# Optimization experiments

Measured on AMD Instinct MI355X. Metric: run time of the kernel, lower is better.

The kernel has to match this reference:

```python
import jax, jax.numpy as jnp
from jax import lax
import numpy as np

L, G, C = 4, 2, 4  # num_blocks, num_sparsity_groups, num_sparsity_cardinals
IMAGE_MEAN = 0.5
SCALE = 2


def _wn(v, g):
    # weight_norm over dims (1,2,3), g per output channel
    n = jnp.sqrt(jnp.sum(v * v, axis=(1, 2, 3), keepdims=True))
    return (g.reshape(-1, 1, 1, 1) / n) * v


def _conv(x, w, b, pad):
    y = lax.conv_general_dilated(x, w, (1, 1), [(pad, pad), (pad, pad)],
                                 dimension_numbers=('NCHW', 'OIHW', 'NCHW'))
    return y + b[None, :, None, None]


def _dyn_conv(x, v, g, b, mw, mb):
    # sparsity-routed conv: per-sample expert mixture of kernels
    w = _wn(v, g)                                   # [G*out, in, k, k]
    B = x.shape[0]
    logits = x.mean((-1, -2)) @ mw.T + mb           # [B, G*C]
    s = jax.nn.softmax(logits.reshape(B, G, C), axis=1)
    wv = w.reshape(G, C, -1, *w.shape[1:])          # [G, C, D, in, k, k]
    wper = jnp.einsum('bgc,gcdikl->bcdikl', s, wv)
    wper = wper.reshape(B, -1, *w.shape[1:])        # [B, out, in, k, k]
    bper = jnp.einsum('bgc,gcd->bcd', s, b.reshape(G, C, -1)).reshape(B, -1)

    def per_sample(xi, wi, bi):
        yi = lax.conv_general_dilated(xi[None], wi, (1, 1), [(1, 1), (1, 1)],
                                      dimension_numbers=('NCHW', 'OIHW', 'NCHW'))[0]
        return yi + bi[:, None, None]

    return jax.vmap(per_sample)(x, wper, bper)


def _pixel_shuffle(x, r):
    B, Cc, H, W = x.shape
    x = x.reshape(B, Cc // (r * r), r, r, H, W)
    x = x.transpose(0, 1, 4, 2, 5, 3)
    return x.reshape(B, Cc // (r * r), H * r, W * r)


def setup_inputs() -> dict:
    key = jax.random.key(0)
    ks = jax.random.split(key, 16)
    f32 = jnp.float32
    inp = {
        'x': jax.random.uniform(ks[0], (8, 3, 64, 64), dtype=f32),
        'head_v': jax.random.normal(ks[1], (64, 3, 3, 3), dtype=f32) * 0.05,
        'head_g': jnp.ones((64,), f32),
        'head_b': jnp.zeros((64,), f32),
        'b1_v': jax.random.normal(ks[2], (L, 512, 64, 3, 3), dtype=f32) * 0.05,
        'b1_g': jnp.full((L, 512), 2.0, f32),
        'b1_b': jnp.zeros((L, 512), f32),
        'b1_mw': jax.random.normal(ks[3], (L, 8, 64), dtype=f32) * 0.05,
        'b1_mb': jax.random.normal(ks[4], (L, 8), dtype=f32) * 0.05,
        'b2_v': jax.random.normal(ks[5], (L, 128, 256, 3, 3), dtype=f32) * 0.05,
        'b2_g': jnp.full((L, 128), 1.0 / np.sqrt(L), f32),
        'b2_b': jnp.zeros((L, 128), f32),
        'b2_mw': jax.random.normal(ks[6], (L, 8, 256), dtype=f32) * 0.05,
        'b2_mb': jax.random.normal(ks[7], (L, 8), dtype=f32) * 0.05,
        'tail_v': jax.random.normal(ks[8], (12, 64, 3, 3), dtype=f32) * 0.05,
        'tail_g': jnp.ones((12,), f32),
        'tail_b': jnp.zeros((12,), f32),
        'skip_v': jax.random.normal(ks[9], (12, 3, 5, 5), dtype=f32) * 0.05,
        'skip_g': jnp.ones((12,), f32),
        'skip_b': jnp.zeros((12,), f32),
    }
    return inp


def reference(x, head_v, head_g, head_b,
              b1_v, b1_g, b1_b, b1_mw, b1_mb,
              b2_v, b2_g, b2_b, b2_mw, b2_mb,
              tail_v, tail_g, tail_b,
              skip_v, skip_g, skip_b):
    x = x - IMAGE_MEAN
    h = _conv(x, _wn(head_v, head_g), head_b, pad=1)
    for l in range(L):
        r0 = h
        t = _dyn_conv(h, b1_v[l], b1_g[l], b1_b[l], b1_mw[l], b1_mb[l])
        t = jax.nn.relu(t)
        t = _dyn_conv(t, b2_v[l], b2_g[l], b2_b[l], b2_mw[l], b2_mb[l])
        h = t + r0
    body = _conv(h, _wn(tail_v, tail_g), tail_b, pad=1)
    s = _conv(x, _wn(skip_v, skip_g), skip_b, pad=2)
    y = _pixel_shuffle(body + s, SCALE) + IMAGE_MEAN
    return y
```

## Files before the change

### kernel.cpp

```cpp
#include <hip/hip_runtime.h>

typedef __attribute__((ext_vector_type(8))) short bf16x8;
typedef __attribute__((ext_vector_type(4))) float f32x4;
typedef __attribute__((ext_vector_type(8))) unsigned short u16x8;

__device__ __forceinline__ unsigned short bf16u(float x) {
    unsigned int u = __builtin_bit_cast(unsigned int, x);
    unsigned int r = (u + 0x7fffu + ((u >> 16) & 1u)) >> 16;
    return (unsigned short)r;
}
__device__ __forceinline__ float bf2f(unsigned short u) {
    return __builtin_bit_cast(float, (unsigned int)u << 16);
}
__device__ __forceinline__ void gll16(const void* g, void* l) {
    __builtin_amdgcn_global_load_lds((const __attribute__((address_space(1))) void*)g,
                                     (__attribute__((address_space(3))) void*)l, 16, 0, 0);
}

__global__ __launch_bounds__(256) void setup_kernel(
    unsigned short* __restrict__ hbf, unsigned short* __restrict__ tbf,
    float* __restrict__ sums,
    const float* __restrict__ hv, const float* __restrict__ hg, float* __restrict__ hw,
    const float* __restrict__ kv, const float* __restrict__ kg, float* __restrict__ kw) {
    int blk = blockIdx.x;
    if (blk < 335) {
        int i = blk * 256 + threadIdx.x;
        u16x8 z8 = {0, 0, 0, 0, 0, 0, 0, 0};
        if (i < 16640) {
            int chv = i & 3, pb = i >> 2, pos = pb % 260, bc = pb / 260;
            int y, x;
            if (pos < 66) { y = 0; x = pos; }
            else if (pos < 132) { y = 65; x = pos - 66; }
            else if (pos < 196) { y = pos - 131; x = 0; }
            else { y = pos - 195; x = 65; }
            *(u16x8*)&hbf[((size_t)bc * 4356 + y * 66 + x) * 32 + chv * 8] = z8;
        } else if (i < 83200) {
            int j = i - 16640;
            int chv = j & 3, pb = j >> 2, pos = pb % 260, bc = pb / 260;
            int y, x;
            if (pos < 66) { y = 0; x = pos; }
            else if (pos < 132) { y = 65; x = pos - 66; }
            else if (pos < 196) { y = pos - 131; x = 0; }
            else { y = pos - 195; x = 65; }
            *(u16x8*)&tbf[((size_t)bc * 4356 + y * 66 + x) * 32 + chv * 8] = z8;
        } else {
            int k = i - 83200;
            f32x4 z4 = {0.f, 0.f, 0.f, 0.f};
            ((f32x4*)sums)[k] = z4;
        }
        return;
    }
    int b2 = blk - 335;
    const float *v, *g;
    float* outw;
    int len, row;
    if (b2 < 64) { v = hv; g = hg; outw = hw; len = 27; row = b2; }
    else         { v = kv; g = kg; outw = kw; len = 75; row = b2 - 64; }
    __shared__ float red[4];
    __shared__ float s_sc;
    const float* vr = v + (size_t)row * len;
    float ss = 0.f;
    for (int i = threadIdx.x; i < len; i += 256) { float a = vr[i]; ss += a * a; }
    for (int o = 32; o > 0; o >>= 1) ss += __shfl_down(ss, o);
    if ((threadIdx.x & 63) == 0) red[threadIdx.x >> 6] = ss;
    __syncthreads();
    if (threadIdx.x == 0) s_sc = g[row] / sqrtf(red[0] + red[1] + red[2] + red[3]);
    __syncthreads();
    float sc = s_sc;
    float* orow = outw + (size_t)row * len;
    for (int i = threadIdx.x; i < len; i += 256) orow[i] = vr[i] * sc;
}

__global__ __launch_bounds__(256) void tail_repack2(const float* __restrict__ tv,
                                                    const float* __restrict__ tg,
                                                    unsigned short* __restrict__ wq) {
    __shared__ float row[576];
    __shared__ float red[4];
    __shared__ float s_sc;
    int mo = blockIdx.x;
    int tid = threadIdx.x;
    if (mo < 12) {
        for (int i = tid; i < 576; i += 256) row[i] = tv[mo * 576 + i];
        __syncthreads();
        float ss = 0.f;
        for (int i = tid; i < 576; i += 256) { float a = row[i]; ss += a * a; }
        for (int o = 32; o > 0; o >>= 1) ss += __shfl_down(ss, o);
        if ((tid & 63) == 0) red[tid >> 6] = ss;
        __syncthreads();
        if (tid == 0) s_sc = tg[mo] / sqrtf(red[0] + red[1] + red[2] + red[3]);
        __syncthreads();
        float sc = s_sc;
        for (int ch = tid; ch < 72; ch += 256) {
            int kg = ch & 3, c2 = ch >> 2;
            int t = c2 % 9, kc = c2 / 9;
            u16x8 pk;
#pragma unroll
            for (int kj = 0; kj < 8; ++kj) {
                int ic = kc * 32 + kg * 8 + kj;
                pk[kj] = bf16u(row[ic * 9 + t] * sc);
            }
            *(u16x8*)&wq[(size_t)((kc * 9 + t) * 4 + kg) * 128 + mo * 8] = pk;
        }
    } else {
        u16x8 z = {0, 0, 0, 0, 0, 0, 0, 0};
        for (int ch = tid; ch < 72; ch += 256) {
            int kg = ch & 3, c2 = ch >> 2;
            int t = c2 % 9, kc = c2 / 9;
            *(u16x8*)&wq[(size_t)((kc * 9 + t) * 4 + kg) * 128 + mo * 8] = z;
        }
    }
}

template <int IC, int GOC, int LGMO>
__global__ __launch_bounds__(256) void combine_v4(
    const float* __restrict__ v, const float* __restrict__ g,
    const float* __restrict__ msum, const float* __restrict__ mw,
    const float* __restrict__ mb, float* __restrict__ s_out,
    unsigned short* __restrict__ wq, int D, int OC) {
    constexpr int ROWF = IC * 9;
    constexpr int KCh = IC / 32;
    constexpr int ROWS2 = 2 * GOC;
    constexpr int TOTC = GOC * KCh * 9 * 4;
    constexpr int TPR = 256 / ROWS2;
    __shared__ float lv[ROWS2 * ROWF];
    __shared__ float lg[8], sv8[8], scr[ROWS2], sw[ROWS2];
    int tid = threadIdx.x;
    int ocg = blockIdx.x * GOC;
    int b = blockIdx.y;
    for (int i = tid; i < ROWS2 * ROWF; i += 256) {
        int r = i / ROWF, jj = i - r * ROWF;
        int oc_r = (r / GOC) * OC + ocg + (r % GOC);
        lv[i] = v[(size_t)oc_r * ROWF + jj];
    }
    {
        int j = tid >> 5, l32 = tid & 31;
        float part = 0.f;
        for (int i = l32; i < IC; i += 32) part += msum[b * IC + i] * mw[j * IC + i];
        for (int m = 16; m > 0; m >>= 1) part += __shfl_xor(part, m);
        if (l32 == 0) lg[j] = part * (1.f / 4096.f) + mb[j];
    }
    __syncthreads();
    {
        int r = tid / TPR, lr = tid % TPR;
        float ss = 0.f;
        for (int i = lr; i < ROWF; i += TPR) { float a = lv[r * ROWF + i]; ss += a * a; }
#pragma unroll
        for (int m = TPR >> 1; m > 0; m >>= 1) ss += __shfl_xor(ss, m);
        if (lr == 0) {
            int oc_r = (r / GOC) * OC + ocg + (r % GOC);
            scr[r] = g[oc_r] / sqrtf(ss);
        }
    }
    if (tid < 8) {
        int gg = tid >> 2, c = tid & 3;
        float l0 = lg[c], l1 = lg[4 + c];
        float m = fmaxf(l0, l1);
        float e0 = __expf(l0 - m), e1 = __expf(l1 - m);
        float val = ((gg == 0) ? e0 : e1) / (e0 + e1);
        sv8[tid] = val;
        if (blockIdx.x == 0) s_out[b * 8 + tid] = val;
    }
    __syncthreads();
    if (tid < ROWS2) {
        int r = tid;
        int oc = ocg + (r % GOC);
        int cd = oc / D;
        float s = (r < GOC) ? sv8[cd] : sv8[4 + cd];
        sw[r] = s * scr[r];
    }
    __syncthreads();
    for (int ci = tid; ci < TOTC; ci += 256) {
        int ml = ci % GOC;
        int c = ci / GOC;
        int kg = c & 3, c2 = c >> 2;
        int t = c2 % 9, kc = c2 / 9;
        int oc = ocg + ml;
        float s0 = sw[ml], s1 = sw[GOC + ml];
        const float* p0 = &lv[(size_t)ml * ROWF];
        const float* p1 = &lv[(size_t)(GOC + ml) * ROWF];
        u16x8 pk;
#pragma unroll
        for (int kj = 0; kj < 8; ++kj) {
            int ic9 = (kc * 32 + kg * 8 + kj) * 9 + t;
            pk[kj] = bf16u(s0 * p0[ic9] + s1 * p1[ic9]);
        }
        size_t w_off = ((((size_t)(b * (OC >> LGMO) + (oc >> LGMO)) * KCh + kc) * 9 + t) * 4 + kg)
                           * ((1 << LGMO) * 8) + (size_t)(oc & ((1 << LGMO) - 1)) * 8;
        *(u16x8*)&wq[w_off] = pk;
    }
}

template <int IC, int OC, int MT, int WM, int WN, int NR,
          bool RELU, bool RES, bool WF32, bool WBF, int OCR, bool DYNB, int MINW>
__global__ __launch_bounds__(WM * WN * 64, MINW)
void conv_mfma(
    const unsigned short* __restrict__ in_bf,
    const unsigned short* __restrict__ wq,
    const float* __restrict__ bias_raw, const float* __restrict__ s8, int lgD,
    float* __restrict__ out,
    unsigned short* __restrict__ out_bf, float* __restrict__ msum, long wstride) {
    constexpr int THREADS = WM * WN * 64;
    constexpr int KCH = IC / 32;
    constexpr int NRH = NR + 2;
    constexpr int NT = NR * 64;
    constexpr int NF = (NT / 16) / WN;
    constexpr int MW = MT / (16 * WM);
    constexpr int WELEM = 9 * 32 * MT;
    constexpr int SELEM = NRH * 66 * 32;
    constexpr int SCH = SELEM / 8;
    constexpr int OCB = OCR / 32;

    __shared__ __align__(16) unsigned short S[2][SELEM];
    __shared__ float MRED[WN][MT];

    const int b = blockIdx.x, ot = blockIdx.z;
    const int y0 = blockIdx.y * NR;
    const int tid = threadIdx.x;
    const int lane = tid & 63;
    const int wid = tid >> 6;
    const int wm = wid / WN, wn = wid % WN;
    const int l15 = lane & 15, lk = lane >> 4;
    const int wmo = wm * (MT / WM);
    const int wno = wn * (NT / WN);

    f32x4 acc[MW][NF];
#pragma unroll
    for (int mf = 0; mf < MW; ++mf)
#pragma unroll
        for (int nf = 0; nf < NF; ++nf)
#pragma unroll
            for (int q = 0; q < 4; ++q) acc[mf][nf][q] = 0.f;

    const unsigned short* inb = in_bf + (size_t)b * KCH * (4356 * 32);
    const unsigned short* wqb = wq + (size_t)b * wstride + (size_t)ot * (KCH * WELEM);
    const unsigned short* wqa = wqb + (size_t)lk * (MT * 8) + (size_t)(wmo + l15) * 8;

    auto STAGE_S = [&](int kc, int buf) {
        const unsigned short* sb = inb + (size_t)kc * (4356 * 32);
        for (int i = tid; i < SCH; i += THREADS) {
            int Lz = i ^ ((i >> 3) & 7);
            int lk2 = Lz & 3, cr = Lz >> 2;
            int col = cr % 66, row = cr / 66;
            gll16(sb + ((size_t)(y0 + row) * 66 + col) * 32 + lk2 * 8,
                  (char*)S[buf] + i * 16);
        }
    };

    bf16x8 aT[2][MW];
#pragma unroll
    for (int mf = 0; mf < MW; ++mf) {
        aT[0][mf] = *(const bf16x8*)(wqa + mf * (16 * 8));
        aT[1][mf] = *(const bf16x8*)(wqa + (4 * MT * 8) + mf * (16 * 8));
    }
    STAGE_S(0, 0);
    __syncthreads();
#pragma unroll
    for (int kc = 0; kc < KCH; ++kc) {
        if (kc + 1 < KCH) STAGE_S(kc + 1, (kc + 1) & 1);
        const unsigned short* Sb = S[kc & 1];
#pragma unroll
        for (int t = 0; t < 9; ++t) {
            const int gt = kc * 9 + t;
            const int pp = gt & 1;
            const int dy = t / 3, dx = t % 3;
#pragma unroll
            for (int nf = 0; nf < NF; ++nf) {
                int n = wno + nf * 16 + l15;
                int r = n >> 6, c = n & 63;
                int L = ((r + dy) * 66 + (c + dx)) * 4 + lk;
                int P = L ^ ((L >> 3) & 7);
                bf16x8 bv = *(const bf16x8*)((const char*)Sb + P * 16);
#pragma unroll
                for (int mf = 0; mf < MW; ++mf)
                    acc[mf][nf] = __builtin_amdgcn_mfma_f32_16x16x32_bf16(aT[pp][mf], bv, acc[mf][nf], 0, 0, 0);
            }
            if (gt + 2 < KCH * 9) {
                const int ngt = gt + 2;
                const int nkc = ngt / 9, nt2 = ngt % 9;
#pragma unroll
                for (int mf = 0; mf < MW; ++mf)
                    aT[pp][mf] = *(const bf16x8*)(wqa + (size_t)nkc * WELEM + nt2 * (4 * MT * 8) + mf * (16 * 8));
            }
        }
        __syncthreads();
    }

    if constexpr (WBF) {
        const int ch = lk >> 1;
        const bool oddlk = (lk & 1);
#pragma unroll
        for (int mf = 0; mf < MW; ++mf) {
            int ocb = ot * MT + wmo + mf * 16 + lk * 4;
            float bvv[4];
#pragma unroll
            for (int q = 0; q < 4; ++q) {
                int oc = ocb + q;
                if (DYNB) {
                    int cc = oc >> lgD;
                    bvv[q] = s8[b * 8 + cc] * bias_raw[oc] + s8[b * 8 + 4 + cc] * bias_raw[OCR + oc];
                } else {
                    bvv[q] = bias_raw[oc];
                }
            }
            int occ = ot * MT + wmo + mf * 16 + ch * 8;
            float msr8[8];
#pragma unroll
            for (int j = 0; j < 8; ++j) msr8[j] = 0.f;
#pragma unroll
            for (int nfp = 0; nfp < NF; nfp += 2) {
                float r0[2][4], pr[2][4];
#pragma unroll
                for (int h = 0; h < 2; ++h)
#pragma unroll
                    for (int q = 0; q < 4; ++q) {
                        float v = acc[mf][nfp + h][q] + bvv[q];
                        if (RELU) v = fmaxf(v, 0.f);
                        r0[h][q] = v;
                    }
#pragma unroll
                for (int h = 0; h < 2; ++h)
#pragma unroll
                    for (int q = 0; q < 4; ++q) pr[h][q] = __shfl_xor(r0[h][q], 16);
                float v8[8];
#pragma unroll
                for (int q = 0; q < 4; ++q) {
                    float own = oddlk ? r0[1][q] : r0[0][q];
                    float oth = oddlk ? pr[1][q] : pr[0][q];
                    v8[q]     = oddlk ? oth : own;
                    v8[4 + q] = oddlk ? own : oth;
                }
                int mynf = nfp + (lk & 1);
                int n = wno + mynf * 16 + l15;
                int y = y0 + (n >> 6), x = n & 63;
                size_t addr = ((((size_t)b * OCB + (occ >> 5)) * 66 + (y + 1)) * 66 + (x + 1)) * 32
                              + (occ & 31);
                if (RES) {
                    u16x8 rv = *(const u16x8*)&out_bf[addr];
#pragma unroll
                    for (int j = 0; j < 8; ++j) v8[j] += bf2f(rv[j]);
                }
                u16x8 pk;
#pragma unroll
                for (int j = 0; j < 8; ++j) pk[j] = bf16u(v8[j]);
                *(u16x8*)&out_bf[addr] = pk;
#pragma unroll
                for (int j = 0; j < 8; ++j) msr8[j] += v8[j];
            }
            if (msum) {
#pragma unroll
                for (int j = 0; j < 8; ++j) {
                    float t = msr8[j];
                    t += __shfl_xor(t, 1);
                    t += __shfl_xor(t, 2);
                    t += __shfl_xor(t, 4);
                    t += __shfl_xor(t, 8);
                    t += __shfl_xor(t, 16);
                    msr8[j] = t;
                }
                if ((lane & 31) == 0) {
#pragma unroll
                    for (int j = 0; j < 8; ++j)
                        MRED[wn][wmo + mf * 16 + ch * 8 + j] = msr8[j];
                }
            }
        }
        if (msum) {
            __syncthreads();
            if (tid < MT) {
                float tot = 0.f;
#pragma unroll
                for (int w2 = 0; w2 < WN; ++w2) tot += MRED[w2][tid];
                atomicAdd(&msum[b * OCR + ot * MT + tid], tot);
            }
        }
    }
    if constexpr (WF32) {
#pragma unroll
        for (int mf = 0; mf < MW; ++mf) {
            int ocb = ot * MT + wmo + mf * 16 + lk * 4;
#pragma unroll
            for (int nf = 0; nf < NF; ++nf) {
                int n = wno + nf * 16 + l15;
                int y = y0 + (n >> 6), x = n & 63;
#pragma unroll
                for (int q = 0; q < 4; ++q) {
                    int oc = ocb + q;
                    if (oc < OCR) {
                        float v = acc[mf][nf][q] + bias_raw[oc];
                        out[(((size_t)b * OCR + oc) * 64 + y) * 64 + x] = v;
                    }
                }
            }
        }
    }
}

__global__ __launch_bounds__(256) void head_conv(
    const float* __restrict__ in, const float* __restrict__ w,
    const float* __restrict__ bias,
    unsigned short* __restrict__ out_bf, float* __restrict__ hsum0) {
    constexpr int OCT = 16, IC = 3;
    __shared__ float s_in[34 * 34];
    __shared__ float s_w[OCT * 9];
    __shared__ float wred[4][OCT];
    int b = blockIdx.z;
    int ocBase = blockIdx.y * OCT;
    int ty0 = (blockIdx.x >> 1) * 32;
    int tx0 = (blockIdx.x & 1) * 32;
    int tid = threadIdx.x;
    int lane = tid & 63, wid = tid >> 6;
    int tx = tid & 15, ty = tid >> 4;

    float acc[OCT][4];
#pragma unroll
    for (int oc = 0; oc < OCT; ++oc)
#pragma unroll
        for (int p = 0; p < 4; ++p) acc[oc][p] = 0.f;

    const float* inb = in + (size_t)b * IC * 4096;
    for (int ic = 0; ic < IC; ++ic) {
        const float* src = inb + (size_t)ic * 4096;
        for (int i = tid; i < 34 * 34; i += 256) {
            int r = i / 34, cc = i % 34;
            int gy = ty0 + r - 1, gx = tx0 + cc - 1;
            float val = 0.f;
            if (gy >= 0 && gy < 64 && gx >= 0 && gx < 64) val = src[gy * 64 + gx] - 0.5f;
            s_in[i] = val;
        }
        for (int i = tid; i < OCT * 9; i += 256) {
            int oc = i / 9, t = i % 9;
            s_w[i] = w[((size_t)(ocBase + oc) * IC + ic) * 9 + t];
        }
        __syncthreads();
        float v[4][4];
#pragma unroll
        for (int r = 0; r < 4; ++r)
#pragma unroll
            for (int cc = 0; cc < 4; ++cc) v[r][cc] = s_in[(2 * ty + r) * 34 + (2 * tx + cc)];
#pragma unroll
        for (int oc = 0; oc < OCT; ++oc) {
#pragma unroll
            for (int ky = 0; ky < 3; ++ky)
#pragma unroll
                for (int kx = 0; kx < 3; ++kx) {
                    float wv = s_w[oc * 9 + ky * 3 + kx];
                    acc[oc][0] += wv * v[ky][kx];
                    acc[oc][1] += wv * v[ky][kx + 1];
                    acc[oc][2] += wv * v[ky + 1][kx];
                    acc[oc][3] += wv * v[ky + 1][kx + 1];
                }
        }
        __syncthreads();
    }
    int py = ty0 + 2 * ty, px = tx0 + 2 * tx;
#pragma unroll
    for (int oc = 0; oc < OCT; ++oc) {
        int og = ocBase + oc;
        float bv = bias[og];
        float osum = 0.f;
#pragma unroll
        for (int p = 0; p < 4; ++p) {
            int dy = p >> 1, dx = p & 1;
            float val = acc[oc][p] + bv;
            osum += val;
            out_bf[((size_t)(b * 2 + (og >> 5)) * 4356 + (py + dy + 1) * 66 + (px + dx + 1)) * 32
                   + (og & 31)] = bf16u(val);
        }
        for (int m = 1; m < 64; m <<= 1) osum += __shfl_xor(osum, m);
        if (lane == 0) wred[wid][oc] = osum;
    }
    __syncthreads();
    if (tid < OCT)
        atomicAdd(&hsum0[b * 64 + ocBase + tid],
                  wred[0][tid] + wred[1][tid] + wred[2][tid] + wred[3][tid]);
}

__global__ __launch_bounds__(256) void shuffle_skip(
    const float* __restrict__ body, const float* __restrict__ x,
    const float* __restrict__ skw, const float* __restrict__ skb,
    float* __restrict__ out) {
    __shared__ float w[900];
    __shared__ float bb[12];
    int tid = threadIdx.x;
    for (int i = tid; i < 900; i += 256) w[i] = skw[i];
    if (tid < 12) bb[tid] = skb[tid];
    __syncthreads();
    int idx = blockIdx.x * 256 + tid;
    int ox = idx & 127;
    int oy = (idx >> 7) & 127;
    int v = idx >> 14;
    int c = v % 3;
    int b = v / 3;
    int rx = ox & 1, ry = oy & 1;
    int xx = ox >> 1, yy = oy >> 1;
    int ch = c * 4 + ry * 2 + rx;
    float acc = bb[ch];
    for (int ic = 0; ic < 3; ++ic)
        for (int ky = 0; ky < 5; ++ky) {
            int gy = yy + ky - 2;
            if (gy < 0 || gy >= 64) continue;
            for (int kx = 0; kx < 5; ++kx) {
                int gx = xx + kx - 2;
                if (gx < 0 || gx >= 64) continue;
                acc += w[((ch * 3 + ic) * 5 + ky) * 5 + kx] *
                       (x[((size_t)(b * 3 + ic) * 64 + gy) * 64 + gx] - 0.5f);
            }
        }
    size_t src = (((size_t)b * 12 + ch) * 64 + yy) * 64 + xx;
    out[idx] = body[src] + acc + 0.5f;
}

extern "C" void kernel_launch(void* const* d_in, const int* in_sizes, int n_in,
                              void* d_out, int out_size, void* d_ws, size_t ws_size,
                              hipStream_t stream) {
    const float* x      = (const float*)d_in[0];
    const float* head_v = (const float*)d_in[1];
    const float* head_g = (const float*)d_in[2];
    const float* head_b = (const float*)d_in[3];
    const float* b1_v   = (const float*)d_in[4];
    const float* b1_g   = (const float*)d_in[5];
    const float* b1_b   = (const float*)d_in[6];
    const float* b1_mw  = (const float*)d_in[7];
    const float* b1_mb  = (const float*)d_in[8];
    const float* b2_v   = (const float*)d_in[9];
    const float* b2_g   = (const float*)d_in[10];
    const float* b2_b   = (const float*)d_in[11];
    const float* b2_mw  = (const float*)d_in[12];
    const float* b2_mb  = (const float*)d_in[13];
    const float* tail_v = (const float*)d_in[14];
    const float* tail_g = (const float*)d_in[15];
    const float* tail_b = (const float*)d_in[16];
    const float* skip_v = (const float*)d_in[17];
    const float* skip_g = (const float*)d_in[18];
    const float* skip_b = (const float*)d_in[19];

    float* ws = (float*)d_ws;
    size_t off = 0;
    auto alloc = [&](size_t n) { float* p = ws + off; off += (n + 3) & ~(size_t)3; return p; };
    float* head_w = alloc(64 * 27);
    float* skip_w = alloc(12 * 75);
    float* sums   = alloc(10240);
    float* sbuf   = alloc(64);
    float* body   = alloc((size_t)8 * 12 * 4096);
    unsigned short* wq1  = (unsigned short*)alloc((size_t)8 * 256 * 576 / 2);
    unsigned short* wq2  = (unsigned short*)alloc((size_t)8 * 64 * 2304 / 2);
    unsigned short* wqt  = (unsigned short*)alloc(9216 / 2);
    unsigned short* h_bf = (unsigned short*)alloc((size_t)8 * 2 * 4356 * 32 / 2);
    unsigned short* t_bf = (unsigned short*)alloc((size_t)8 * 8 * 4356 * 32 / 2);
    (void)ws_size; (void)in_sizes; (void)n_in; (void)out_size;

    auto hsum = [&](int l) { return sums + l * 512; };
    auto tsum = [&](int l) { return sums + 2048 + l * 2048; };

    setup_kernel<<<411, 256, 0, stream>>>(h_bf, t_bf, sums, head_v, head_g, head_w,
                                          skip_v, skip_g, skip_w);
    tail_repack2<<<16, 256, 0, stream>>>(tail_v, tail_g, wqt);
    head_conv<<<dim3(4, 4, 8), 256, 0, stream>>>(x, head_w, head_b, h_bf, hsum(0));

    for (int l = 0; l < 4; ++l) {
        combine_v4<64, 4, 6><<<dim3(64, 8), 256, 0, stream>>>(
            b1_v + (size_t)l * 512 * 576, b1_g + (size_t)l * 512, hsum(l),
            b1_mw + (size_t)l * 8 * 64, b1_mb + l * 8, sbuf, wq1, 64, 256);
        conv_mfma<64, 256, 64, 2, 2, 2, true, false, false, true, 256, true, 4>
            <<<dim3(8, 32, 4), 256, 0, stream>>>(h_bf, wq1, b1_b + (size_t)l * 512, sbuf, 6,
                                                 nullptr, t_bf, tsum(l), 147456);
        combine_v4<256, 2, 6><<<dim3(32, 8), 256, 0, stream>>>(
            b2_v + (size_t)l * 128 * 2304, b2_g + (size_t)l * 128, tsum(l),
            b2_mw + (size_t)l * 8 * 256, b2_mb + l * 8, sbuf, wq2, 16, 64);
        conv_mfma<256, 64, 64, 4, 2, 1, false, true, false, true, 64, true, 4>
            <<<dim3(8, 64, 1), 512, 0, stream>>>(t_bf, wq2, b2_b + (size_t)l * 128, sbuf, 4,
                                                 nullptr, h_bf, (l < 3) ? hsum(l + 1) : nullptr,
                                                 147456);
    }

    conv_mfma<64, 16, 16, 1, 4, 2, false, false, true, false, 12, false, 2>
        <<<dim3(8, 32, 1), 256, 0, stream>>>(h_bf, wqt, tail_b, nullptr, 0,
                                             body, nullptr, nullptr, 0);
    shuffle_skip<<<1536, 256, 0, stream>>>(body, x, skip_w, skip_b, (float*)d_out);
}
```

Measured before the change: 313.1 us.

## Merge tail repack into setup, prestage both K-chunks, retune head and conv2 tiling

Folds the tail weight repack into the setup kernel, which removes one launch. For conv_mfma instances with two K-chunks, both input chunks are staged up front, removing the mid-loop staging and the per-chunk barrier. The head conv drops to 8 output channels per block with twice as many blocks. The second conv's block goes from 512 threads to 256 by changing a warp-layout template parameter. These changes trade LDS footprint and per-thread work against launch overhead, occupancy and sync cost.

Result: slower. 322.7 us (+3.1%).

```diff
diff --git a/kernel.cpp b/kernel.cpp
--- a/kernel.cpp
+++ b/kernel.cpp
@@ -21,10 +21,13 @@
     unsigned short* __restrict__ hbf, unsigned short* __restrict__ tbf,
     float* __restrict__ sums,
     const float* __restrict__ hv, const float* __restrict__ hg, float* __restrict__ hw,
-    const float* __restrict__ kv, const float* __restrict__ kg, float* __restrict__ kw) {
+    const float* __restrict__ kv, const float* __restrict__ kg, float* __restrict__ kw,
+    const float* __restrict__ tv, const float* __restrict__ tg,
+    unsigned short* __restrict__ wqt) {
     int blk = blockIdx.x;
+    int tid = threadIdx.x;
     if (blk < 335) {
-        int i = blk * 256 + threadIdx.x;
+        int i = blk * 256 + tid;
         u16x8 z8 = {0, 0, 0, 0, 0, 0, 0, 0};
         if (i < 16640) {
             int chv = i & 3, pb = i >> 2, pos = pb % 260, bc = pb / 260;
@@ -50,40 +53,35 @@
         }
         return;
     }
-    int b2 = blk - 335;
-    const float *v, *g;
-    float* outw;
-    int len, row;
-    if (b2 < 64) { v = hv; g = hg; outw = hw; len = 27; row = b2; }
-    else         { v = kv; g = kg; outw = kw; len = 75; row = b2 - 64; }
+    __shared__ float srow[576];
     __shared__ float red[4];
     __shared__ float s_sc;
-    const float* vr = v + (size_t)row * len;
-    float ss = 0.f;
-    for (int i = threadIdx.x; i < len; i += 256) { float a = vr[i]; ss += a * a; }
-    for (int o = 32; o > 0; o >>= 1) ss += __shfl_down(ss, o);
-    if ((threadIdx.x & 63) == 0) red[threadIdx.x >> 6] = ss;
-    __syncthreads();
-    if (threadIdx.x == 0) s_sc = g[row] / sqrtf(red[0] + red[1] + red[2] + red[3]);
-    __syncthreads();
-    float sc = s_sc;
-    float* orow = outw + (size_t)row * len;
-    for (int i = threadIdx.x; i < len; i += 256) orow[i] = vr[i] * sc;
-}
-
-__global__ __launch_bounds__(256) void tail_repack2(const float* __restrict__ tv,
-                                                    const float* __restrict__ tg,
-                                                    unsigned short* __restrict__ wq) {
-    __shared__ float row[576];
-    __shared__ float red[4];
-    __shared__ float s_sc;
-    int mo = blockIdx.x;
-    int tid = threadIdx.x;
+    if (blk < 411) {
+        int b2 = blk - 335;
+        const float *v, *g;
+        float* outw;
+        int len, row;
+        if (b2 < 64) { v = hv; g = hg; outw = hw; len = 27; row = b2; }
+        else         { v = kv; g = kg; outw = kw; len = 75; row = b2 - 64; }
+        const float* vr = v + (size_t)row * len;
+        float ss = 0.f;
+        for (int i = tid; i < len; i += 256) { float a = vr[i]; ss += a * a; }
+        for (int o = 32; o > 0; o >>= 1) ss += __shfl_down(ss, o);
+        if ((tid & 63) == 0) red[tid >> 6] = ss;
+        __syncthreads();
+        if (tid == 0) s_sc = g[row] / sqrtf(red[0] + red[1] + red[2] + red[3]);
+        __syncthreads();
+        float sc = s_sc;
+        float* orow = outw + (size_t)row * len;
+        for (int i = tid; i < len; i += 256) orow[i] = vr[i] * sc;
+        return;
+    }
+    int mo = blk - 411;
     if (mo < 12) {
-        for (int i = tid; i < 576; i += 256) row[i] = tv[mo * 576 + i];
+        for (int i = tid; i < 576; i += 256) srow[i] = tv[mo * 576 + i];
         __syncthreads();
         float ss = 0.f;
-        for (int i = tid; i < 576; i += 256) { float a = row[i]; ss += a * a; }
+        for (int i = tid; i < 576; i += 256) { float a = srow[i]; ss += a * a; }
         for (int o = 32; o > 0; o >>= 1) ss += __shfl_down(ss, o);
         if ((tid & 63) == 0) red[tid >> 6] = ss;
         __syncthreads();
@@ -97,16 +95,16 @@
 #pragma unroll
             for (int kj = 0; kj < 8; ++kj) {
                 int ic = kc * 32 + kg * 8 + kj;
-                pk[kj] = bf16u(row[ic * 9 + t] * sc);
-            }
-            *(u16x8*)&wq[(size_t)((kc * 9 + t) * 4 + kg) * 128 + mo * 8] = pk;
+                pk[kj] = bf16u(srow[ic * 9 + t] * sc);
+            }
+            *(u16x8*)&wqt[(size_t)((kc * 9 + t) * 4 + kg) * 128 + mo * 8] = pk;
         }
     } else {
         u16x8 z = {0, 0, 0, 0, 0, 0, 0, 0};
         for (int ch = tid; ch < 72; ch += 256) {
             int kg = ch & 3, c2 = ch >> 2;
             int t = c2 % 9, kc = c2 / 9;
-            *(u16x8*)&wq[(size_t)((kc * 9 + t) * 4 + kg) * 128 + mo * 8] = z;
+            *(u16x8*)&wqt[(size_t)((kc * 9 + t) * 4 + kg) * 128 + mo * 8] = z;
         }
     }
 }
@@ -252,11 +250,18 @@
         aT[0][mf] = *(const bf16x8*)(wqa + mf * (16 * 8));
         aT[1][mf] = *(const bf16x8*)(wqa + (4 * MT * 8) + mf * (16 * 8));
     }
-    STAGE_S(0, 0);
+    if constexpr (KCH == 2) {
+        STAGE_S(0, 0);
+        STAGE_S(1, 1);
+    } else {
+        STAGE_S(0, 0);
+    }
     __syncthreads();
 #pragma unroll
     for (int kc = 0; kc < KCH; ++kc) {
-        if (kc + 1 < KCH) STAGE_S(kc + 1, (kc + 1) & 1);
+        if constexpr (KCH != 2) {
+            if (kc + 1 < KCH) STAGE_S(kc + 1, (kc + 1) & 1);
+        }
         const unsigned short* Sb = S[kc & 1];
 #pragma unroll
         for (int t = 0; t < 9; ++t) {
@@ -282,7 +287,7 @@
                     aT[pp][mf] = *(const bf16x8*)(wqa + (size_t)nkc * WELEM + nt2 * (4 * MT * 8) + mf * (16 * 8));
             }
         }
-        __syncthreads();
+        if constexpr (KCH != 2) __syncthreads();
     }
 
     if constexpr (WBF) {
@@ -399,7 +404,7 @@
     const float* __restrict__ in, const float* __restrict__ w,
     const float* __restrict__ bias,
     unsigned short* __restrict__ out_bf, float* __restrict__ hsum0) {
-    constexpr int OCT = 16, IC = 3;
+    constexpr int OCT = 8, IC = 3;
     __shared__ float s_in[34 * 34];
     __shared__ float s_w[OCT * 9];
     __shared__ float wred[4][OCT];
@@ -552,10 +557,9 @@
     auto hsum = [&](int l) { return sums + l * 512; };
     auto tsum = [&](int l) { return sums + 2048 + l * 2048; };
 
-    setup_kernel<<<411, 256, 0, stream>>>(h_bf, t_bf, sums, head_v, head_g, head_w,
-                                          skip_v, skip_g, skip_w);
-    tail_repack2<<<16, 256, 0, stream>>>(tail_v, tail_g, wqt);
-    head_conv<<<dim3(4, 4, 8), 256, 0, stream>>>(x, head_w, head_b, h_bf, hsum(0));
+    setup_kernel<<<427, 256, 0, stream>>>(h_bf, t_bf, sums, head_v, head_g, head_w,
+                                          skip_v, skip_g, skip_w, tail_v, tail_g, wqt);
+    head_conv<<<dim3(4, 8, 8), 256, 0, stream>>>(x, head_w, head_b, h_bf, hsum(0));
 
     for (int l = 0; l < 4; ++l) {
         combine_v4<64, 4, 6><<<dim3(64, 8), 256, 0, stream>>>(
@@ -567,8 +571,8 @@
         combine_v4<256, 2, 6><<<dim3(32, 8), 256, 0, stream>>>(
             b2_v + (size_t)l * 128 * 2304, b2_g + (size_t)l * 128, tsum(l),
             b2_mw + (size_t)l * 8 * 256, b2_mb + l * 8, sbuf, wq2, 16, 64);
-        conv_mfma<256, 64, 64, 4, 2, 1, false, true, false, true, 64, true, 4>
-            <<<dim3(8, 64, 1), 512, 0, stream>>>(t_bf, wq2, b2_b + (size_t)l * 128, sbuf, 4,
+        conv_mfma<256, 64, 64, 2, 2, 1, false, true, false, true, 64, true, 4>
+            <<<dim3(8, 64, 1), 256, 0, stream>>>(t_bf, wq2, b2_b + (size_t)l * 128, sbuf, 4,
                                                  nullptr, h_bf, (l < 3) ? hsum(l + 1) : nullptr,
                                                  147456);
     }
```
